# Performance work log

Hardware: AMD Instinct MI355X
Metric: run time of the kernel (lower is better)

Reference implementation:

```python
import jax, jax.numpy as jnp
import numpy as np

EPS = 1e-5

def dwconv(x, w):
    # x: (B,C,T), w: (C,1,3) depthwise, stride 1, pad 1
    return jax.lax.conv_general_dilated(
        x, w, window_strides=(1,), padding=[(1, 1)],
        dimension_numbers=('NCH', 'OIH', 'NCH'),
        feature_group_count=x.shape[1])

def chan_ln(x, w, b):
    # LayerNorm over channel dim (axis=1) of (B,C,T)
    mu = jnp.mean(x, axis=1, keepdims=True)
    r = x - mu
    sigma = jnp.mean(r * r, axis=1, keepdims=True)
    return (r / jnp.sqrt(sigma + EPS)) * w + b

def conv1x1(x, w, b):
    # x: (B,C,T), w: (O,C), b: (O,)
    return jnp.einsum('oc,bct->bot', w, x) + b[None, :, None]

def setup_inputs() -> dict:
    B, C, T, H = 4, 1024, 1024, 16
    key0 = jax.random.key(0)
    ks = jax.random.split(key0, 16)
    s = 0.02
    inp = {
        'query': jax.random.normal(ks[0], (B, C, T), jnp.float32),
        'key': jax.random.normal(ks[1], (B, C, T), jnp.float32),
        'value': jax.random.normal(ks[2], (B, C, T), jnp.float32),
        'query_mask': jnp.ones((B, 1, T), jnp.bool_),
        'kv_mask': jnp.ones((B, 1, T), jnp.bool_),
        # depthwise conv weights (C,1,3), no bias
        'qconv_w': jax.random.normal(ks[3], (C, 1, 3), jnp.float32) * s,
        'kconv_w': jax.random.normal(ks[4], (C, 1, 3), jnp.float32) * s,
        'vconv_w': jax.random.normal(ks[5], (C, 1, 3), jnp.float32) * s,
        # channel LayerNorm affine params (1,C,1)
        'qn_w': jnp.ones((1, C, 1), jnp.float32), 'qn_b': jnp.zeros((1, C, 1), jnp.float32),
        'kn_w': jnp.ones((1, C, 1), jnp.float32), 'kn_b': jnp.zeros((1, C, 1), jnp.float32),
        'vn_w': jnp.ones((1, C, 1), jnp.float32), 'vn_b': jnp.zeros((1, C, 1), jnp.float32),
        # 1x1 conv (= per-timestep linear) weights (C,C) + bias (C,)
        'wq': jax.random.normal(ks[6], (C, C), jnp.float32) * s, 'bq': jnp.zeros((C,), jnp.float32),
        'wk': jax.random.normal(ks[7], (C, C), jnp.float32) * s, 'bk': jnp.zeros((C,), jnp.float32),
        'wv': jax.random.normal(ks[8], (C, C), jnp.float32) * s, 'bv': jnp.zeros((C,), jnp.float32),
        'wp': jax.random.normal(ks[9], (C, C), jnp.float32) * s, 'bp': jnp.zeros((C,), jnp.float32),
    }
    return inp

def reference(query, key, value, query_mask, kv_mask,
              qconv_w, kconv_w, vconv_w,
              qn_w, qn_b, kn_w, kn_b, vn_w, vn_b,
              wq, bq, wk, bk, wv, bv, wp, bp):
    B, C, T = query.shape
    H = 16
    ch = C // H
    scale = 1.0 / jnp.sqrt(jnp.asarray(ch, query.dtype))
    qm = query_mask.astype(query.dtype)   # (B,1,T), stride 1 -> qx_mask == query_mask
    kvm = kv_mask.astype(query.dtype)

    q = chan_ln(dwconv(query, qconv_w) * qm, qn_w, qn_b)
    k = chan_ln(dwconv(key, kconv_w) * kvm, kn_w, kn_b)
    v = chan_ln(dwconv(value, vconv_w) * kvm, vn_w, vn_b)

    q = conv1x1(q, wq, bq)
    k = conv1x1(k, wk, bk)
    v = conv1x1(v, wv, bv)

    # (B,C,T) -> (B,H,T,ch)
    q = q.reshape(B, H, ch, T).transpose(0, 1, 3, 2)
    k = k.reshape(B, H, ch, T).transpose(0, 1, 3, 2)
    v = v.reshape(B, H, ch, T).transpose(0, 1, 3, 2)

    att = jax.nn.softmax(jnp.einsum('bhsc,bhtc->bhst', q, k) * scale, axis=-1)
    # post-softmax mask applied to V (not to scores) — faithful to the original
    vm = v * kvm[:, :, :, None]           # (B,1,T)->(B,1,T,1) broadcast over heads/ch
    out = jnp.einsum('bhst,bhtc->bhsc', att, vm)

    out = out.transpose(0, 1, 3, 2).reshape(B, C, T)
    out = conv1x1(out, wp, bp) * qm
    return out, query_mask
```

## Files before the change

kernel.cpp:

```cpp
#include <hip/hip_runtime.h>
#include <math.h>

#define B_ 4
#define C_ 1024
#define T_ 1024
#define H_ 16
#define CH_ 64
#define BCT (B_ * C_ * T_)

typedef __attribute__((ext_vector_type(8))) short s16x8;
typedef __attribute__((ext_vector_type(4))) float f32x4;
typedef unsigned short u16;

#define MFMA16(a, b, c) __builtin_amdgcn_mfma_f32_16x16x32_bf16((a), (b), (c), 0, 0, 0)

extern "C" __device__ float __ocml_native_exp2_f32(float);

__device__ __forceinline__ u16 f2bf(float f) {
    union { float f; unsigned u; } v; v.f = f;
    unsigned r = (v.u + 0x7fffu + ((v.u >> 16) & 1u)) >> 16;
    return (u16)r;
}
__device__ __forceinline__ float bf2f(u16 h) {
    union { unsigned u; float f; } v; v.u = (unsigned)h << 16; return v.f;
}

typedef __attribute__((address_space(3))) unsigned int lds_u32;
typedef __attribute__((address_space(1))) const unsigned int glb_u32;
__device__ __forceinline__ void glds16(const void* g, const void* l_wave_uniform) {
    __builtin_amdgcn_global_load_lds(
        (glb_u32*)(unsigned long long)g,
        (lds_u32*)(unsigned long long)l_wave_uniform, 16, 0, 0);
}

#define WAIT_BARRIER(N)                                   \
    asm volatile("s_waitcnt vmcnt(" #N ")" ::: "memory"); \
    __builtin_amdgcn_s_barrier();                         \
    __builtin_amdgcn_sched_barrier(0)

__global__ __launch_bounds__(512) void prep_kernel(
    const float* __restrict__ xq, const float* __restrict__ xk, const float* __restrict__ xv,
    const float* __restrict__ wq3, const float* __restrict__ wk3, const float* __restrict__ wv3,
    const int* __restrict__ qm, const int* __restrict__ kvm,
    const float* __restrict__ qnw, const float* __restrict__ qnb,
    const float* __restrict__ knw, const float* __restrict__ knb,
    const float* __restrict__ vnw, const float* __restrict__ vnb,
    u16* __restrict__ oq, u16* __restrict__ ok, u16* __restrict__ ov,
    const float* __restrict__ w0, const float* __restrict__ w1,
    const float* __restrict__ w2, const float* __restrict__ w3,
    u16* __restrict__ o0, u16* __restrict__ o1, u16* __restrict__ o2, u16* __restrict__ o3,
    float* __restrict__ tail_out, int ntail)
{
    __shared__ __align__(16) u16 tile[32 * 1032];
    __shared__ float red1[16][33], red2[16][33];
    __shared__ float musL[32], rssL[32];

    const int bid = blockIdx.x;
    if (bid >= 384) {
        if (bid >= 2432) {
            int i = (bid - 2432) * 512 + threadIdx.x;
            if (i < ntail) tail_out[i] = (qm[i] != 0) ? 1.f : 0.f;
            return;
        }
        const int b2 = bid - 384;
        const int mat = b2 >> 9;
        const float* __restrict__ w = (mat == 0) ? w0 : (mat == 1) ? w1 : (mat == 2) ? w2 : w3;
        u16* __restrict__ o = (mat == 0) ? o0 : (mat == 1) ? o1 : (mat == 2) ? o2 : o3;
        const int i = ((b2 & 511) * 512 + threadIdx.x) * 4;
        float4 v = *(const float4*)&w[i];
        uint2 p;
        p.x = (unsigned)f2bf(v.x) | ((unsigned)f2bf(v.y) << 16);
        p.y = (unsigned)f2bf(v.z) | ((unsigned)f2bf(v.w) << 16);
        *(uint2*)&o[i] = p;
        return;
    }

    const int z = bid >> 5;
    const int tensor = z >> 2, b = z & 3;
    const float* __restrict__ x   = (tensor == 0) ? xq  : (tensor == 1) ? xk  : xv;
    const float* __restrict__ w3c = (tensor == 0) ? wq3 : (tensor == 1) ? wk3 : wv3;
    const int* __restrict__ msk   = (tensor == 0) ? qm  : kvm;
    const float* __restrict__ wln = (tensor == 0) ? qnw : (tensor == 1) ? knw : vnw;
    const float* __restrict__ bln = (tensor == 0) ? qnb : (tensor == 1) ? knb : vnb;
    u16* __restrict__ xt = (tensor == 0) ? oq : (tensor == 1) ? ok : ov;

    const int t0 = (bid & 31) * 32;

    const int tl = threadIdx.x & 31, cs = threadIdx.x >> 5;
    const int t = t0 + tl;
    const float mk = (msk[b * T_ + t] != 0) ? 1.f : 0.f;

    float s1 = 0.f, s2 = 0.f;
    #pragma unroll 4
    for (int i = 0; i < 32; ++i) {
        const int c = 2 * (cs + 16 * i);
        const float* xr0 = x + ((size_t)(b * C_ + c)) * T_ + t;
        const float* xr1 = xr0 + T_;
        float xc0 = xr0[0];
        float xm0 = (t > 0)      ? xr0[-1] : 0.f;
        float xp0 = (t < T_ - 1) ? xr0[1]  : 0.f;
        float v0 = (w3c[3 * c + 0] * xm0 + w3c[3 * c + 1] * xc0 + w3c[3 * c + 2] * xp0) * mk;
        float xc1 = xr1[0];
        float xm1 = (t > 0)      ? xr1[-1] : 0.f;
        float xp1 = (t < T_ - 1) ? xr1[1]  : 0.f;
        float v1 = (w3c[3 * c + 3] * xm1 + w3c[3 * c + 4] * xc1 + w3c[3 * c + 5] * xp1) * mk;
        s1 += v0 + v1;
        s2 += v0 * v0 + v1 * v1;
        *(unsigned*)&tile[tl * 1032 + c] =
            (unsigned)f2bf(v0) | ((unsigned)f2bf(v1) << 16);
    }
    red1[cs][tl] = s1;
    red2[cs][tl] = s2;
    __syncthreads();
    if (threadIdx.x < 32) {
        float a = 0.f, q2 = 0.f;
        #pragma unroll
        for (int i = 0; i < 16; ++i) { a += red1[i][threadIdx.x]; q2 += red2[i][threadIdx.x]; }
        float m_  = a  * (1.f / C_);
        float var = q2 * (1.f / C_) - m_ * m_;
        musL[threadIdx.x] = m_;
        rssL[threadIdx.x] = rsqrtf(var + 1e-5f);
    }
    __syncthreads();

    #pragma unroll
    for (int it = 0; it < 8; ++it) {
        const int idx = it * 512 + threadIdx.x;
        const int tt = idx >> 7, c0 = (idx & 127) * 8;
        const s16x8 pv = *(const s16x8*)&tile[tt * 1032 + c0];
        const float m_ = musL[tt], rv = rssL[tt];
        const float4 w0v = *(const float4*)&wln[c0];
        const float4 w1v = *(const float4*)&wln[c0 + 4];
        const float4 b0v = *(const float4*)&bln[c0];
        const float4 b1v = *(const float4*)&bln[c0 + 4];
        uint4 o;
        float f0, f1;
        f0 = (bf2f((u16)pv[0]) - m_) * rv * w0v.x + b0v.x;
        f1 = (bf2f((u16)pv[1]) - m_) * rv * w0v.y + b0v.y;
        o.x = (unsigned)f2bf(f0) | ((unsigned)f2bf(f1) << 16);
        f0 = (bf2f((u16)pv[2]) - m_) * rv * w0v.z + b0v.z;
        f1 = (bf2f((u16)pv[3]) - m_) * rv * w0v.w + b0v.w;
        o.y = (unsigned)f2bf(f0) | ((unsigned)f2bf(f1) << 16);
        f0 = (bf2f((u16)pv[4]) - m_) * rv * w1v.x + b1v.x;
        f1 = (bf2f((u16)pv[5]) - m_) * rv * w1v.y + b1v.y;
        o.z = (unsigned)f2bf(f0) | ((unsigned)f2bf(f1) << 16);
        f0 = (bf2f((u16)pv[6]) - m_) * rv * w1v.z + b1v.z;
        f1 = (bf2f((u16)pv[7]) - m_) * rv * w1v.w + b1v.w;
        o.w = (unsigned)f2bf(f0) | ((unsigned)f2bf(f1) << 16);
        *(uint4*)&xt[((size_t)(b * T_ + t0 + tt)) * C_ + c0] = o;
    }
}

__device__ __forceinline__ void stage_slab(
    const u16* __restrict__ gA, const u16* __restrict__ gB,
    u16* lA, u16* lB, int k0, int wave, int lane)
{
    const int rw = lane >> 2, ch = lane & 3;
    const int sw = ((ch ^ ((rw >> 1) & 3)) * 8) + k0;
    const int r0 = 16 * wave + rw, r1 = r0 + 64;
    glds16(gA + (size_t)r0 * C_ + sw, lA + (16 * wave) * 32);
    glds16(gA + (size_t)r1 * C_ + sw, lA + (64 + 16 * wave) * 32);
    glds16(gB + (size_t)r0 * C_ + sw, lB + (16 * wave) * 32);
    glds16(gB + (size_t)r1 * C_ + sw, lB + (64 + 16 * wave) * 32);
}

template<int OUT_BF16>
__device__ __forceinline__ void gemm_core(
    const u16* __restrict__ A, const u16* __restrict__ B, void* __restrict__ D,
    const float* __restrict__ bias, const int* __restrict__ mask,
    float scale, int bias_on_n, int m0, int n0)
{
    __shared__ __align__(16) u16 As[3][128 * 32];
    __shared__ __align__(16) u16 Bs[3][128 * 32];
    const int tid = threadIdx.x, lane = tid & 63, wave = tid >> 6;
    const int r = lane & 15, g = lane >> 4;
    const int wm = (wave >> 1) * 64, wn = (wave & 1) * 64;
    const u16* Ab = A + (size_t)m0 * C_;
    const u16* Bb = B + (size_t)n0 * C_;

    f32x4 acc[4][4];
    #pragma unroll
    for (int i = 0; i < 4; ++i)
        #pragma unroll
        for (int j = 0; j < 4; ++j) acc[i][j] = f32x4{0.f, 0.f, 0.f, 0.f};

    stage_slab(Ab, Bb, As[0], Bs[0], 0, wave, lane);
    stage_slab(Ab, Bb, As[1], Bs[1], 32, wave, lane);
    WAIT_BARRIER(4);

    const int swz = (g ^ ((r >> 1) & 3)) * 8;
    const int NK = C_ / 32;
    int cur = 0;
    for (int kk = 0; kk < NK; ++kk) {
        int pre = cur + 2; if (pre >= 3) pre -= 3;
        if (kk + 2 < NK)
            stage_slab(Ab, Bb, As[pre], Bs[pre], (kk + 2) * 32, wave, lane);
        s16x8 af[4], bf[4];
        #pragma unroll
        for (int mi = 0; mi < 4; ++mi)
            af[mi] = *(const s16x8*)&As[cur][(wm + 16 * mi + r) * 32 + swz];
        #pragma unroll
        for (int ni = 0; ni < 4; ++ni)
            bf[ni] = *(const s16x8*)&Bs[cur][(wn + 16 * ni + r) * 32 + swz];
        #pragma unroll
        for (int mi = 0; mi < 4; ++mi)
            #pragma unroll
            for (int ni = 0; ni < 4; ++ni)
                acc[mi][ni] = MFMA16(af[mi], bf[ni], acc[mi][ni]);
        if (kk + 1 < NK) {
            if (kk + 2 < NK) { WAIT_BARRIER(4); }
            else             { WAIT_BARRIER(0); }
        }
        cur = (cur == 2) ? 0 : cur + 1;
    }

    #pragma unroll
    for (int mi = 0; mi < 4; ++mi) {
        #pragma unroll
        for (int ni = 0; ni < 4; ++ni) {
            const int n = n0 + wn + 16 * ni + r;
            float mk = 1.f;
            if (mask) mk = (mask[n] != 0) ? 1.f : 0.f;
            #pragma unroll
            for (int i = 0; i < 4; ++i) {
                const int m = m0 + wm + 16 * mi + 4 * g + i;
                float v = acc[mi][ni][i] + (bias_on_n ? bias[n] : bias[m]);
                v *= scale * mk;
                size_t o = (size_t)m * 1024 + n;
                if (OUT_BF16) ((u16*)D)[o] = f2bf(v);
                else          ((float*)D)[o] = v;
            }
        }
    }
}

__global__ __launch_bounds__(256) void gemm_qkv_kernel(
    const u16* __restrict__ Xq, const u16* __restrict__ Xk, const u16* __restrict__ Xv,
    const u16* __restrict__ Wq, const u16* __restrict__ Wk, const u16* __restrict__ Wv,
    const float* __restrict__ bq, const float* __restrict__ bk, const float* __restrict__ bv,
    u16* __restrict__ Qt, u16* __restrict__ Kt, u16* __restrict__ Vb, const int* __restrict__ kvm)
{
    const int p = blockIdx.x;
    const int lb = (p & 7) * 96 + (p >> 3);
    const int z = lb >> 6, yy = (lb >> 3) & 7, xx = lb & 7;
    const int tensor = z >> 2, b = z & 3;
    const size_t off = (size_t)b * (1024 * 1024);
    const float qscale = 0.125f * 1.44269504088896340736f;
    const u16* A = (tensor == 0) ? Xq + off : (tensor == 1) ? Xk + off : Wv;
    const u16* B = (tensor == 0) ? Wq       : (tensor == 1) ? Wk       : Xv + off;
    u16*       D = (tensor == 0) ? Qt + off : (tensor == 1) ? Kt + off : Vb + off;
    const float* bias = (tensor == 0) ? bq : (tensor == 1) ? bk : bv;
    const int* mask = (tensor == 2) ? kvm + (size_t)b * T_ : nullptr;
    gemm_core<1>(A, B, D, bias, mask, (tensor == 0) ? qscale : 1.f, tensor != 2,
                 yy * 128, xx * 128);
}

__global__ __launch_bounds__(256) void gemm_out_kernel(
    const u16* __restrict__ Wp, const u16* __restrict__ att,
    const float* __restrict__ bp, float* __restrict__ out, const int* __restrict__ qm)
{
    const int p = blockIdx.x;
    const int lb = (p & 7) * 32 + (p >> 3);
    const int b = lb >> 6, yy = (lb >> 3) & 7, xx = lb & 7;
    const size_t off = (size_t)b * (1024 * 1024);
    gemm_core<0>(Wp, att + off, out + off, bp, qm + (size_t)b * T_, 1.f, 0,
                 yy * 128, xx * 128);
}

__global__ __launch_bounds__(256) void attn_mfma_kernel(
    const u16* __restrict__ Qt, const u16* __restrict__ Kt, const u16* __restrict__ Vb,
    u16* __restrict__ att)
{
    const int p = blockIdx.x;
    const int lb = (p & 7) * 64 + (p >> 3);
    const int bh = lb >> 3, sblk = lb & 7;
    const int b = bh >> 4, h = bh & 15;
    const int lane = threadIdx.x & 63, wave = threadIdx.x >> 6;
    const int r = lane & 15, g = lane >> 4;
    const int hofs = h * 64;
    const int s0 = sblk * 128 + wave * 16;

    __shared__ __align__(16) u16 Ks[3][64 * 64];
    __shared__ __align__(16) u16 Vs[3][64 * 64];
    __shared__ __align__(16) u16 P_lds[4][2][16 * 72];

    const u16* qb0 = Qt + ((size_t)(b * T_ + s0 + r)) * C_ + hofs + g * 8;
    const s16x8 qf00 = *(const s16x8*)(qb0);
    const s16x8 qf01 = *(const s16x8*)(qb0 + 32);
    const s16x8 qf10 = *(const s16x8*)(qb0 + (size_t)64 * C_);
    const s16x8 qf11 = *(const s16x8*)(qb0 + (size_t)64 * C_ + 32);

    const int srow = lane >> 3, sch = lane & 7;
    const u16* kg = Kt + ((size_t)(b * T_)) * C_ + hofs;
    const u16* vg = Vb + ((size_t)(b * C_ + hofs)) * T_;

    auto stage = [&](int buf, int t0) {
        #pragma unroll
        for (int i = 0; i < 2; ++i) {
            const int rr = 16 * wave + 8 * i + srow;
            const int sw = (sch ^ (rr & 7)) * 8;
            glds16(kg + (size_t)(t0 + rr) * C_ + sw, &Ks[buf][(16 * wave + 8 * i) * 64]);
            glds16(vg + (size_t)rr * T_ + t0 + sw,   &Vs[buf][(16 * wave + 8 * i) * 64]);
        }
    };

    f32x4 acc0[4], acc1[4];
    #pragma unroll
    for (int ci = 0; ci < 4; ++ci) {
        acc0[ci] = f32x4{0.f, 0.f, 0.f, 0.f};
        acc1[ci] = f32x4{0.f, 0.f, 0.f, 0.f};
    }
    float l0 = 0.f, l1 = 0.f;
    u16* pw0 = &P_lds[wave][0][0];
    u16* pw1 = &P_lds[wave][1][0];

    stage(0, 0);
    stage(1, 64);
    WAIT_BARRIER(4);

    const int NT = T_ / 64;
    int cur = 0;
    for (int it = 0; it < NT; ++it) {
        int pre = cur + 2; if (pre >= 3) pre -= 3;
        if (it + 2 < NT) stage(pre, (it + 2) * 64);

        const u16* ks = Ks[cur];
        f32x4 st0[4], st1[4];
        __builtin_amdgcn_s_setprio(1);
        #pragma unroll
        for (int tt = 0; tt < 4; ++tt) {
            const int row = (16 * tt + r) * 64;
            const s16x8 ka = *(const s16x8*)&ks[row + ((g ^ (r & 7)) * 8)];
            const s16x8 kb = *(const s16x8*)&ks[row + (((4 + g) ^ (r & 7)) * 8)];
            f32x4 sa = f32x4{0.f, 0.f, 0.f, 0.f};
            sa = MFMA16(ka, qf00, sa); sa = MFMA16(kb, qf01, sa); st0[tt] = sa;
            f32x4 sb = f32x4{0.f, 0.f, 0.f, 0.f};
            sb = MFMA16(ka, qf10, sb); sb = MFMA16(kb, qf11, sb); st1[tt] = sb;
        }
        __builtin_amdgcn_s_setprio(0);

        #pragma unroll
        for (int tt = 0; tt < 4; ++tt) {
            float a0 = __ocml_native_exp2_f32(st0[tt][0]);
            float a1 = __ocml_native_exp2_f32(st0[tt][1]);
            float a2 = __ocml_native_exp2_f32(st0[tt][2]);
            float a3 = __ocml_native_exp2_f32(st0[tt][3]);
            l0 += (a0 + a1) + (a2 + a3);
            uint2 pk;
            pk.x = (unsigned)f2bf(a0) | ((unsigned)f2bf(a1) << 16);
            pk.y = (unsigned)f2bf(a2) | ((unsigned)f2bf(a3) << 16);
            *(uint2*)&pw0[r * 72 + 16 * tt + 4 * g] = pk;
            float b0 = __ocml_native_exp2_f32(st1[tt][0]);
            float b1 = __ocml_native_exp2_f32(st1[tt][1]);
            float b2 = __ocml_native_exp2_f32(st1[tt][2]);
            float b3 = __ocml_native_exp2_f32(st1[tt][3]);
            l1 += (b0 + b1) + (b2 + b3);
            pk.x = (unsigned)f2bf(b0) | ((unsigned)f2bf(b1) << 16);
            pk.y = (unsigned)f2bf(b2) | ((unsigned)f2bf(b3) << 16);
            *(uint2*)&pw1[r * 72 + 16 * tt + 4 * g] = pk;
        }

        const u16* vs = Vs[cur];
        __builtin_amdgcn_s_setprio(1);
        #pragma unroll
        for (int kk = 0; kk < 2; ++kk) {
            const s16x8 pa0 = *(const s16x8*)&pw0[r * 72 + 32 * kk + 8 * g];
            const s16x8 pa1 = *(const s16x8*)&pw1[r * 72 + 32 * kk + 8 * g];
            #pragma unroll
            for (int ci = 0; ci < 4; ++ci) {
                const s16x8 vf = *(const s16x8*)
                    &vs[(16 * ci + r) * 64 + (((4 * kk + g) ^ (r & 7)) * 8)];
                acc0[ci] = MFMA16(pa0, vf, acc0[ci]);
                acc1[ci] = MFMA16(pa1, vf, acc1[ci]);
            }
        }
        __builtin_amdgcn_s_setprio(0);

        if (it + 1 < NT) {
            if (it + 2 < NT) { WAIT_BARRIER(4); }
            else             { WAIT_BARRIER(0); }
        }
        cur = (cur == 2) ? 0 : cur + 1;
    }

    l0 += __shfl_xor(l0, 16); l0 += __shfl_xor(l0, 32);
    l1 += __shfl_xor(l1, 16); l1 += __shfl_xor(l1, 32);
    const float inv0 = 1.f / l0, inv1 = 1.f / l1;
    const float i00 = __shfl(inv0, 4 * g + 0), i01 = __shfl(inv0, 4 * g + 1);
    const float i02 = __shfl(inv0, 4 * g + 2), i03 = __shfl(inv0, 4 * g + 3);
    const float i10 = __shfl(inv1, 4 * g + 0), i11 = __shfl(inv1, 4 * g + 1);
    const float i12 = __shfl(inv1, 4 * g + 2), i13 = __shfl(inv1, 4 * g + 3);

    u16* ob = att + ((size_t)(b * T_ + s0 + 4 * g)) * C_ + hofs + r;
    #pragma unroll
    for (int ci = 0; ci < 4; ++ci) {
        ob[(size_t)0 * C_ + ci * 16] = f2bf(acc0[ci][0] * i00);
        ob[(size_t)1 * C_ + ci * 16] = f2bf(acc0[ci][1] * i01);
        ob[(size_t)2 * C_ + ci * 16] = f2bf(acc0[ci][2] * i02);
        ob[(size_t)3 * C_ + ci * 16] = f2bf(acc0[ci][3] * i03);
    }
    u16* ob1 = ob + (size_t)64 * C_;
    #pragma unroll
    for (int ci = 0; ci < 4; ++ci) {
        ob1[(size_t)0 * C_ + ci * 16] = f2bf(acc1[ci][0] * i10);
        ob1[(size_t)1 * C_ + ci * 16] = f2bf(acc1[ci][1] * i11);
        ob1[(size_t)2 * C_ + ci * 16] = f2bf(acc1[ci][2] * i12);
        ob1[(size_t)3 * C_ + ci * 16] = f2bf(acc1[ci][3] * i13);
    }
}

extern "C" void kernel_launch(void* const* d_in, const int* in_sizes, int n_in,
                              void* d_out, int out_size, void* d_ws, size_t ws_size,
                              hipStream_t stream)
{
    const float* query = (const float*)d_in[0];
    const float* key_  = (const float*)d_in[1];
    const float* value = (const float*)d_in[2];
    const int* qm  = (const int*)d_in[3];
    const int* kvm = (const int*)d_in[4];
    const float* qconv = (const float*)d_in[5];
    const float* kconv = (const float*)d_in[6];
    const float* vconv = (const float*)d_in[7];
    const float* qnw = (const float*)d_in[8];
    const float* qnb = (const float*)d_in[9];
    const float* knw = (const float*)d_in[10];
    const float* knb = (const float*)d_in[11];
    const float* vnw = (const float*)d_in[12];
    const float* vnb = (const float*)d_in[13];
    const float* wq = (const float*)d_in[14];
    const float* bq = (const float*)d_in[15];
    const float* wk = (const float*)d_in[16];
    const float* bk = (const float*)d_in[17];
    const float* wv = (const float*)d_in[18];
    const float* bv = (const float*)d_in[19];
    const float* wp = (const float*)d_in[20];
    const float* bp = (const float*)d_in[21];

    const size_t MB = 1024 * 1024;
    char* W = (char*)d_ws;
    u16* Xq  = (u16*)(W + 0 * MB);
    u16* Xk  = (u16*)(W + 8 * MB);
    u16* Xv  = (u16*)(W + 16 * MB);
    u16* Qt  = (u16*)(W + 24 * MB);
    u16* Kt  = (u16*)(W + 32 * MB);
    u16* Vb_ = (u16*)(W + 40 * MB);
    u16* att_ = (u16*)(W + 48 * MB);
    u16* wqb = (u16*)(W + 56 * MB);
    u16* wkb = (u16*)(W + 58 * MB);
    u16* wvb = (u16*)(W + 60 * MB);
    u16* wpb = (u16*)(W + 62 * MB);

    int ntail = out_size - BCT;
    if (ntail < 0) ntail = 0;

    prep_kernel<<<dim3(2440), 512, 0, stream>>>(
        query, key_, value, qconv, kconv, vconv, qm, kvm,
        qnw, qnb, knw, knb, vnw, vnb, Xq, Xk, Xv,
        wq, wk, wv, wp, wqb, wkb, wvb, wpb,
        (float*)d_out + BCT, ntail);

    gemm_qkv_kernel<<<dim3(768), 256, 0, stream>>>(
        Xq, Xk, Xv, wqb, wkb, wvb, bq, bk, bv, Qt, Kt, Vb_, kvm);

    attn_mfma_kernel<<<dim3(512), 256, 0, stream>>>(Qt, Kt, Vb_, att_);

    gemm_out_kernel<<<dim3(256), 256, 0, stream>>>(wpb, att_, bp, (float*)d_out, qm);
}
```

Baseline: 119.6 us.

## Use FP8 e4m3 operands for the QKV projection GEMM

The prep kernel now writes the normalized activations and the Q/K/V weights (pre-scaled by 64) as FP8 e4m3 instead of bf16. A dedicated QKV GEMM kernel uses the fp8 16x16x32 MFMA with byte-sized LDS slabs and rescales by 1/64 in the epilogue. This halves the operand bytes read and staged and uses the faster FP8 matrix path, at the cost of lower precision in the projections. The output GEMM keeps bf16 and is inlined into its own kernel.

```diff
diff --git a/kernel.cpp b/kernel.cpp
--- a/kernel.cpp
+++ b/kernel.cpp
@@ -11,8 +11,10 @@
 typedef __attribute__((ext_vector_type(8))) short s16x8;
 typedef __attribute__((ext_vector_type(4))) float f32x4;
 typedef unsigned short u16;
+typedef unsigned char u8;
 
 #define MFMA16(a, b, c) __builtin_amdgcn_mfma_f32_16x16x32_bf16((a), (b), (c), 0, 0, 0)
+#define MFMA8(a, b, c)  __builtin_amdgcn_mfma_f32_16x16x32_fp8_fp8((a), (b), (c), 0, 0, 0)
 
 extern "C" __device__ float __ocml_native_exp2_f32(float);
 
@@ -23,6 +25,21 @@
 }
 __device__ __forceinline__ float bf2f(u16 h) {
     union { unsigned u; float f; } v; v.u = (unsigned)h << 16; return v.f;
+}
+
+__device__ __forceinline__ u8 f2e4m3(float x) {
+    union { float f; unsigned u; } v; v.f = x;
+    const unsigned s = (v.u >> 24) & 0x80;
+    const float a = fabsf(x);
+    if (a >= 448.f) return (u8)(s | 0x7E);
+    if (a < 0.03125f) {
+        int n = (int)rintf(a * 512.f);
+        return (u8)(s | (unsigned)n);
+    }
+    unsigned u = v.u & 0x7fffffff;
+    unsigned r = u + 0x7FFFF + ((u >> 20) & 1);
+    unsigned e8 = (r >> 23) - 120;
+    return (u8)(s | (e8 << 3) | ((r >> 20) & 7));
 }
 
 typedef __attribute__((address_space(3))) unsigned int lds_u32;
@@ -45,10 +62,10 @@
     const float* __restrict__ qnw, const float* __restrict__ qnb,
     const float* __restrict__ knw, const float* __restrict__ knb,
     const float* __restrict__ vnw, const float* __restrict__ vnb,
-    u16* __restrict__ oq, u16* __restrict__ ok, u16* __restrict__ ov,
+    u8* __restrict__ oq, u8* __restrict__ ok, u8* __restrict__ ov,
     const float* __restrict__ w0, const float* __restrict__ w1,
     const float* __restrict__ w2, const float* __restrict__ w3,
-    u16* __restrict__ o0, u16* __restrict__ o1, u16* __restrict__ o2, u16* __restrict__ o3,
+    u8* __restrict__ o0, u8* __restrict__ o1, u8* __restrict__ o2, u16* __restrict__ o3,
     float* __restrict__ tail_out, int ntail)
 {
     __shared__ __align__(16) u16 tile[32 * 1032];
@@ -64,14 +81,23 @@
         }
         const int b2 = bid - 384;
         const int mat = b2 >> 9;
-        const float* __restrict__ w = (mat == 0) ? w0 : (mat == 1) ? w1 : (mat == 2) ? w2 : w3;
-        u16* __restrict__ o = (mat == 0) ? o0 : (mat == 1) ? o1 : (mat == 2) ? o2 : o3;
         const int i = ((b2 & 511) * 512 + threadIdx.x) * 4;
-        float4 v = *(const float4*)&w[i];
-        uint2 p;
-        p.x = (unsigned)f2bf(v.x) | ((unsigned)f2bf(v.y) << 16);
-        p.y = (unsigned)f2bf(v.z) | ((unsigned)f2bf(v.w) << 16);
-        *(uint2*)&o[i] = p;
+        if (mat == 3) {
+            float4 v = *(const float4*)&w3[i];
+            uint2 p;
+            p.x = (unsigned)f2bf(v.x) | ((unsigned)f2bf(v.y) << 16);
+            p.y = (unsigned)f2bf(v.z) | ((unsigned)f2bf(v.w) << 16);
+            *(uint2*)&o3[i] = p;
+        } else {
+            const float* __restrict__ w = (mat == 0) ? w0 : (mat == 1) ? w1 : w2;
+            u8* __restrict__ o = (mat == 0) ? o0 : (mat == 1) ? o1 : o2;
+            float4 v = *(const float4*)&w[i];
+            unsigned pk = (unsigned)f2e4m3(64.f * v.x)
+                        | ((unsigned)f2e4m3(64.f * v.y) << 8)
+                        | ((unsigned)f2e4m3(64.f * v.z) << 16)
+                        | ((unsigned)f2e4m3(64.f * v.w) << 24);
+            *(unsigned*)&o[i] = pk;
+        }
         return;
     }
 
@@ -82,7 +108,7 @@
     const int* __restrict__ msk   = (tensor == 0) ? qm  : kvm;
     const float* __restrict__ wln = (tensor == 0) ? qnw : (tensor == 1) ? knw : vnw;
     const float* __restrict__ bln = (tensor == 0) ? qnb : (tensor == 1) ? knb : vnb;
-    u16* __restrict__ xt = (tensor == 0) ? oq : (tensor == 1) ? ok : ov;
+    u8* __restrict__ xt = (tensor == 0) ? oq : (tensor == 1) ? ok : ov;
 
     const int t0 = (bid & 31) * 32;
 
@@ -129,25 +155,110 @@
         const int tt = idx >> 7, c0 = (idx & 127) * 8;
         const s16x8 pv = *(const s16x8*)&tile[tt * 1032 + c0];
         const float m_ = musL[tt], rv = rssL[tt];
-        const float4 w0v = *(const float4*)&wln[c0];
-        const float4 w1v = *(const float4*)&wln[c0 + 4];
-        const float4 b0v = *(const float4*)&bln[c0];
-        const float4 b1v = *(const float4*)&bln[c0 + 4];
-        uint4 o;
-        float f0, f1;
-        f0 = (bf2f((u16)pv[0]) - m_) * rv * w0v.x + b0v.x;
-        f1 = (bf2f((u16)pv[1]) - m_) * rv * w0v.y + b0v.y;
-        o.x = (unsigned)f2bf(f0) | ((unsigned)f2bf(f1) << 16);
-        f0 = (bf2f((u16)pv[2]) - m_) * rv * w0v.z + b0v.z;
-        f1 = (bf2f((u16)pv[3]) - m_) * rv * w0v.w + b0v.w;
-        o.y = (unsigned)f2bf(f0) | ((unsigned)f2bf(f1) << 16);
-        f0 = (bf2f((u16)pv[4]) - m_) * rv * w1v.x + b1v.x;
-        f1 = (bf2f((u16)pv[5]) - m_) * rv * w1v.y + b1v.y;
-        o.z = (unsigned)f2bf(f0) | ((unsigned)f2bf(f1) << 16);
-        f0 = (bf2f((u16)pv[6]) - m_) * rv * w1v.z + b1v.z;
-        f1 = (bf2f((u16)pv[7]) - m_) * rv * w1v.w + b1v.w;
-        o.w = (unsigned)f2bf(f0) | ((unsigned)f2bf(f1) << 16);
-        *(uint4*)&xt[((size_t)(b * T_ + t0 + tt)) * C_ + c0] = o;
+        float fv[8];
+        #pragma unroll
+        for (int j = 0; j < 8; ++j)
+            fv[j] = (bf2f((u16)pv[j]) - m_) * rv * wln[c0 + j] + bln[c0 + j];
+        uint2 o;
+        o.x = (unsigned)f2e4m3(fv[0]) | ((unsigned)f2e4m3(fv[1]) << 8)
+            | ((unsigned)f2e4m3(fv[2]) << 16) | ((unsigned)f2e4m3(fv[3]) << 24);
+        o.y = (unsigned)f2e4m3(fv[4]) | ((unsigned)f2e4m3(fv[5]) << 8)
+            | ((unsigned)f2e4m3(fv[6]) << 16) | ((unsigned)f2e4m3(fv[7]) << 24);
+        *(uint2*)&xt[((size_t)(b * T_ + t0 + tt)) * C_ + c0] = o;
+    }
+}
+
+__device__ __forceinline__ void stage_slab8(
+    const u8* __restrict__ gA, const u8* __restrict__ gB,
+    u8* lA, u8* lB, int k0, int wave, int lane)
+{
+    const int rl = lane >> 1, h = lane & 1;
+    const int row = wave * 32 + rl;
+    const int hs = (h ^ ((row >> 2) & 1)) * 16;
+    glds16(gA + (size_t)row * C_ + k0 + hs, lA + wave * 1024);
+    glds16(gB + (size_t)row * C_ + k0 + hs, lB + wave * 1024);
+}
+
+__global__ __launch_bounds__(256) void gemm_qkv_kernel(
+    const u8* __restrict__ Xq, const u8* __restrict__ Xk, const u8* __restrict__ Xv,
+    const u8* __restrict__ Wq, const u8* __restrict__ Wk, const u8* __restrict__ Wv,
+    const float* __restrict__ bq, const float* __restrict__ bk, const float* __restrict__ bv,
+    u16* __restrict__ Qt, u16* __restrict__ Kt, u16* __restrict__ Vb, const int* __restrict__ kvm)
+{
+    const int p = blockIdx.x;
+    const int lb = (p & 7) * 96 + (p >> 3);
+    const int z = lb >> 6, yy = (lb >> 3) & 7, xx = lb & 7;
+    const int tensor = z >> 2, b = z & 3;
+    const size_t off = (size_t)b * (1024 * 1024);
+    const float qscale = 0.125f * 1.44269504088896340736f;
+    const u8* A = (tensor == 0) ? Xq + off : (tensor == 1) ? Xk + off : Wv;
+    const u8* B = (tensor == 0) ? Wq       : (tensor == 1) ? Wk       : Xv + off;
+    u16*     D = (tensor == 0) ? Qt + off : (tensor == 1) ? Kt + off : Vb + off;
+    const float* bias = (tensor == 0) ? bq : (tensor == 1) ? bk : bv;
+    const int* mask = (tensor == 2) ? kvm + (size_t)b * T_ : nullptr;
+    const float scale = (tensor == 0) ? qscale : 1.f;
+    const int bias_on_n = (tensor != 2);
+    const int m0 = yy * 128, n0 = xx * 128;
+
+    __shared__ __align__(16) u8 As[3][128 * 32];
+    __shared__ __align__(16) u8 Bs[3][128 * 32];
+    const int tid = threadIdx.x, lane = tid & 63, wave = tid >> 6;
+    const int r = lane & 15, g = lane >> 4;
+    const int wm = (wave >> 1) * 64, wn = (wave & 1) * 64;
+    const u8* Ab = A + (size_t)m0 * C_;
+    const u8* Bb = B + (size_t)n0 * C_;
+
+    f32x4 acc[4][4];
+    #pragma unroll
+    for (int i = 0; i < 4; ++i)
+        #pragma unroll
+        for (int j = 0; j < 4; ++j) acc[i][j] = f32x4{0.f, 0.f, 0.f, 0.f};
+
+    stage_slab8(Ab, Bb, As[0], Bs[0], 0, wave, lane);
+    stage_slab8(Ab, Bb, As[1], Bs[1], 32, wave, lane);
+    WAIT_BARRIER(2);
+
+    const int rsw = ((r >> 2) & 1) << 1;
+    const int NK = C_ / 32;
+    int cur = 0;
+    for (int kk = 0; kk < NK; ++kk) {
+        int pre = cur + 2; if (pre >= 3) pre -= 3;
+        if (kk + 2 < NK)
+            stage_slab8(Ab, Bb, As[pre], Bs[pre], (kk + 2) * 32, wave, lane);
+        long af[4], bf[4];
+        #pragma unroll
+        for (int mi = 0; mi < 4; ++mi)
+            af[mi] = *(const long*)&As[cur][(wm + 16 * mi + r) * 32 + ((g ^ rsw) * 8)];
+        #pragma unroll
+        for (int ni = 0; ni < 4; ++ni)
+            bf[ni] = *(const long*)&Bs[cur][(wn + 16 * ni + r) * 32 + ((g ^ rsw) * 8)];
+        #pragma unroll
+        for (int mi = 0; mi < 4; ++mi)
+            #pragma unroll
+            for (int ni = 0; ni < 4; ++ni)
+                acc[mi][ni] = MFMA8(af[mi], bf[ni], acc[mi][ni]);
+        if (kk + 1 < NK) {
+            if (kk + 2 < NK) { WAIT_BARRIER(2); }
+            else             { WAIT_BARRIER(0); }
+        }
+        cur = (cur == 2) ? 0 : cur + 1;
+    }
+
+    #pragma unroll
+    for (int mi = 0; mi < 4; ++mi) {
+        #pragma unroll
+        for (int ni = 0; ni < 4; ++ni) {
+            const int n = n0 + wn + 16 * ni + r;
+            float mk = 1.f;
+            if (mask) mk = (mask[n] != 0) ? 1.f : 0.f;
+            #pragma unroll
+            for (int i = 0; i < 4; ++i) {
+                const int m = m0 + wm + 16 * mi + 4 * g + i;
+                float v = acc[mi][ni][i] * 0.015625f + (bias_on_n ? bias[n] : bias[m]);
+                v *= scale * mk;
+                D[(size_t)m * 1024 + n] = f2bf(v);
+            }
+        }
     }
 }
 
@@ -164,19 +275,25 @@
     glds16(gB + (size_t)r1 * C_ + sw, lB + (64 + 16 * wave) * 32);
 }
 
-template<int OUT_BF16>
-__device__ __forceinline__ void gemm_core(
-    const u16* __restrict__ A, const u16* __restrict__ B, void* __restrict__ D,
-    const float* __restrict__ bias, const int* __restrict__ mask,
-    float scale, int bias_on_n, int m0, int n0)
-{
+__global__ __launch_bounds__(256) void gemm_out_kernel(
+    const u16* __restrict__ Wp, const u16* __restrict__ att,
+    const float* __restrict__ bp, float* __restrict__ out, const int* __restrict__ qm)
+{
+    const int p = blockIdx.x;
+    const int lb = (p & 7) * 32 + (p >> 3);
+    const int b = lb >> 6, yy = (lb >> 3) & 7, xx = lb & 7;
+    const size_t off = (size_t)b * (1024 * 1024);
+    const int m0 = yy * 128, n0 = xx * 128;
+    const u16* Ab = Wp + (size_t)m0 * C_;
+    const u16* Bb = att + off + (size_t)n0 * C_;
+    float* D = out + off;
+    const int* mask = qm + (size_t)b * T_;
+
     __shared__ __align__(16) u16 As[3][128 * 32];
     __shared__ __align__(16) u16 Bs[3][128 * 32];
     const int tid = threadIdx.x, lane = tid & 63, wave = tid >> 6;
     const int r = lane & 15, g = lane >> 4;
     const int wm = (wave >> 1) * 64, wn = (wave & 1) * 64;
-    const u16* Ab = A + (size_t)m0 * C_;
-    const u16* Bb = B + (size_t)n0 * C_;
 
     f32x4 acc[4][4];
     #pragma unroll
@@ -219,52 +336,15 @@
         #pragma unroll
         for (int ni = 0; ni < 4; ++ni) {
             const int n = n0 + wn + 16 * ni + r;
-            float mk = 1.f;
-            if (mask) mk = (mask[n] != 0) ? 1.f : 0.f;
+            const float mk = (mask[n] != 0) ? 1.f : 0.f;
             #pragma unroll
             for (int i = 0; i < 4; ++i) {
                 const int m = m0 + wm + 16 * mi + 4 * g + i;
-                float v = acc[mi][ni][i] + (bias_on_n ? bias[n] : bias[m]);
-                v *= scale * mk;
-                size_t o = (size_t)m * 1024 + n;
-                if (OUT_BF16) ((u16*)D)[o] = f2bf(v);
-                else          ((float*)D)[o] = v;
+                float v = (acc[mi][ni][i] + bp[m]) * mk;
+                D[(size_t)m * 1024 + n] = v;
             }
         }
     }
-}
-
-__global__ __launch_bounds__(256) void gemm_qkv_kernel(
-    const u16* __restrict__ Xq, const u16* __restrict__ Xk, const u16* __restrict__ Xv,
-    const u16* __restrict__ Wq, const u16* __restrict__ Wk, const u16* __restrict__ Wv,
-    const float* __restrict__ bq, const float* __restrict__ bk, const float* __restrict__ bv,
-    u16* __restrict__ Qt, u16* __restrict__ Kt, u16* __restrict__ Vb, const int* __restrict__ kvm)
-{
-    const int p = blockIdx.x;
-    const int lb = (p & 7) * 96 + (p >> 3);
-    const int z = lb >> 6, yy = (lb >> 3) & 7, xx = lb & 7;
-    const int tensor = z >> 2, b = z & 3;
-    const size_t off = (size_t)b * (1024 * 1024);
-    const float qscale = 0.125f * 1.44269504088896340736f;
-    const u16* A = (tensor == 0) ? Xq + off : (tensor == 1) ? Xk + off : Wv;
-    const u16* B = (tensor == 0) ? Wq       : (tensor == 1) ? Wk       : Xv + off;
-    u16*       D = (tensor == 0) ? Qt + off : (tensor == 1) ? Kt + off : Vb + off;
-    const float* bias = (tensor == 0) ? bq : (tensor == 1) ? bk : bv;
-    const int* mask = (tensor == 2) ? kvm + (size_t)b * T_ : nullptr;
-    gemm_core<1>(A, B, D, bias, mask, (tensor == 0) ? qscale : 1.f, tensor != 2,
-                 yy * 128, xx * 128);
-}
-
-__global__ __launch_bounds__(256) void gemm_out_kernel(
-    const u16* __restrict__ Wp, const u16* __restrict__ att,
-    const float* __restrict__ bp, float* __restrict__ out, const int* __restrict__ qm)
-{
-    const int p = blockIdx.x;
-    const int lb = (p & 7) * 32 + (p >> 3);
-    const int b = lb >> 6, yy = (lb >> 3) & 7, xx = lb & 7;
-    const size_t off = (size_t)b * (1024 * 1024);
-    gemm_core<0>(Wp, att + off, out + off, bp, qm + (size_t)b * T_, 1.f, 0,
-                 yy * 128, xx * 128);
 }
 
 __global__ __launch_bounds__(256) void attn_mfma_kernel(
@@ -438,16 +518,16 @@
 
     const size_t MB = 1024 * 1024;
     char* W = (char*)d_ws;
-    u16* Xq  = (u16*)(W + 0 * MB);
-    u16* Xk  = (u16*)(W + 8 * MB);
-    u16* Xv  = (u16*)(W + 16 * MB);
+    u8* Xq   = (u8*)(W + 0 * MB);
+    u8* Xk   = (u8*)(W + 8 * MB);
+    u8* Xv   = (u8*)(W + 16 * MB);
     u16* Qt  = (u16*)(W + 24 * MB);
     u16* Kt  = (u16*)(W + 32 * MB);
     u16* Vb_ = (u16*)(W + 40 * MB);
     u16* att_ = (u16*)(W + 48 * MB);
-    u16* wqb = (u16*)(W + 56 * MB);
-    u16* wkb = (u16*)(W + 58 * MB);
-    u16* wvb = (u16*)(W + 60 * MB);
+    u8* wq8  = (u8*)(W + 56 * MB);
+    u8* wk8  = (u8*)(W + 58 * MB);
+    u8* wv8  = (u8*)(W + 60 * MB);
     u16* wpb = (u16*)(W + 62 * MB);
 
     int ntail = out_size - BCT;
@@ -456,11 +536,11 @@
     prep_kernel<<<dim3(2440), 512, 0, stream>>>(
         query, key_, value, qconv, kconv, vconv, qm, kvm,
         qnw, qnb, knw, knb, vnw, vnb, Xq, Xk, Xv,
-        wq, wk, wv, wp, wqb, wkb, wvb, wpb,
+        wq, wk, wv, wp, wq8, wk8, wv8, wpb,
         (float*)d_out + BCT, ntail);
 
     gemm_qkv_kernel<<<dim3(768), 256, 0, stream>>>(
-        Xq, Xk, Xv, wqb, wkb, wvb, bq, bk, bv, Qt, Kt, Vb_, kvm);
+        Xq, Xk, Xv, wq8, wk8, wv8, bq, bk, bv, Qt, Kt, Vb_, kvm);
 
     attn_mfma_kernel<<<dim3(512), 256, 0, stream>>>(Qt, Kt, Vb_, att_);
 
```

Measured after the change: 122.2 us. 1.02x slower.
